# Performance work log

Measured on AMD Instinct MI355X. Metric: run time of the kernel, lower is better.

Reference implementation:

```python
import jax, jax.numpy as jnp
import numpy as np

TOP_K = 2  # num_active_experts


def setup_inputs() -> dict:
    key = jax.random.key(0)
    k1, k2, k3 = jax.random.split(key, 3)
    N, D, E = 16384, 1024, 8
    x = jax.random.normal(k1, (N, D), dtype=jnp.float32)
    router_w = jax.random.normal(k2, (E, D), dtype=jnp.float32) * (1.0 / np.sqrt(D))
    router_b = jnp.zeros((E,), dtype=jnp.float32)
    expert_w = jax.random.normal(k3, (E, D, D), dtype=jnp.float32) * (1.0 / np.sqrt(D))
    expert_b = jnp.zeros((E, D), dtype=jnp.float32)
    return {"x": x, "router_w": router_w, "router_b": router_b,
            "expert_w": expert_w, "expert_b": expert_b}


def reference(x, router_w, router_b, expert_w, expert_b):
    E = router_w.shape[0]
    # Router: softmax over experts, pick top-k, renormalize
    logits = x @ router_w.T + router_b                      # [N, E]
    probs = jax.nn.softmax(logits, axis=-1)                 # [N, E]
    top_p, top_i = jax.lax.top_k(probs, TOP_K)              # [N, K]
    top_p = top_p / jnp.sum(top_p, axis=-1, keepdims=True)  # renormalized gates
    # Dense combine weights: [N, E], zero for non-selected experts
    combine = jnp.sum(jax.nn.one_hot(top_i, E, dtype=x.dtype) * top_p[..., None], axis=1)
    # All-expert outputs, then weighted combine (vectorized dispatch/combine)
    y = jnp.einsum('nd,eod->neo', x, expert_w) + expert_b   # [N, E, O]
    out = jnp.einsum('neo,ne->no', y, combine)              # [N, O]
    return out
```

## Files before the change

kernel.cpp:

```cpp
#include <hip/hip_runtime.h>
#include <hip/hip_bf16.h>


constexpr int DIMS = 1024;
constexpr int NE   = 8;
constexpr int ROUTER_BLOCKS = 1024;
constexpr int WCONV_BLOCKS  = NE * DIMS * DIMS / (8 * 256);

typedef __attribute__((ext_vector_type(8))) short short8;
typedef __attribute__((ext_vector_type(4))) float f32x4;

typedef const __attribute__((address_space(1))) void* gp_t;
typedef __attribute__((address_space(3))) void* sp_t;

__device__ __forceinline__ float b2f(unsigned short u) {
  union { unsigned int i; float f; } x; x.i = ((unsigned)u) << 16; return x.f;
}

__global__ __launch_bounds__(256) void prep_kernel(
    const float* __restrict__ x, const float* __restrict__ rw,
    const float* __restrict__ rb, const float* __restrict__ ew,
    __hip_bfloat16* __restrict__ xb, __hip_bfloat16* __restrict__ wb,
    int* __restrict__ counts, int* __restrict__ entries,
    float* __restrict__ gates, int n_tok) {
  const int tid = threadIdx.x;

  if ((int)blockIdx.x >= ROUTER_BLOCKS) {
    size_t i = (size_t)(blockIdx.x - ROUTER_BLOCKS) * 256 + tid;
    const float4* w4 = (const float4*)ew;
    float4 a = w4[i * 2], b = w4[i * 2 + 1];
    union { __hip_bfloat16 h[8]; float4 f; } u;
    u.h[0] = __float2bfloat16(a.x); u.h[1] = __float2bfloat16(a.y);
    u.h[2] = __float2bfloat16(a.z); u.h[3] = __float2bfloat16(a.w);
    u.h[4] = __float2bfloat16(b.x); u.h[5] = __float2bfloat16(b.y);
    u.h[6] = __float2bfloat16(b.z); u.h[7] = __float2bfloat16(b.w);
    ((float4*)wb)[i] = u.f;
    return;
  }

  __shared__ float s_rw[NE * DIMS];
  __shared__ int s_cnt[NE], s_base[NE];
  __shared__ int s_e[32];
  __shared__ float s_g[32];
  __shared__ int s_pos[32];

  const float4* rw4 = (const float4*)rw;
  float4* s4 = (float4*)s_rw;
  for (int i = tid; i < NE * DIMS / 4; i += 256) s4[i] = rw4[i];
  if (tid < NE) s_cnt[tid] = 0;
  __syncthreads();

  const int wave = tid >> 6, lane = tid & 63;
  for (int i = 0; i < 4; ++i) {
    int t = blockIdx.x * 16 + wave * 4 + i;
    float a[NE];
#pragma unroll
    for (int e = 0; e < NE; ++e) a[e] = 0.f;
#pragma unroll
    for (int j = 0; j < DIMS / 64; ++j) {
      int d = lane + j * 64;
      float v = x[(size_t)t * DIMS + d];
      xb[(size_t)t * DIMS + d] = __float2bfloat16(v);
#pragma unroll
      for (int e = 0; e < NE; ++e) a[e] = fmaf(v, s_rw[e * DIMS + d], a[e]);
    }
    double da[NE];
#pragma unroll
    for (int e = 0; e < NE; ++e) da[e] = (double)a[e];
#pragma unroll
    for (int off = 32; off > 0; off >>= 1) {
#pragma unroll
      for (int e = 0; e < NE; ++e) da[e] += __shfl_xor(da[e], off, 64);
    }
    if (lane == 0) {
      float l[NE];
#pragma unroll
      for (int e = 0; e < NE; ++e) l[e] = (float)da[e] + rb[e];
      int e0 = 0;
#pragma unroll
      for (int e = 1; e < NE; ++e) if (l[e] > l[e0]) e0 = e;
      int e1 = (e0 == 0) ? 1 : 0;
#pragma unroll
      for (int e = 0; e < NE; ++e) if (e != e0 && l[e] > l[e1]) e1 = e;
      float r = expf(l[e1] - l[e0]);
      float g0 = 1.f / (1.f + r);
      float g1 = 1.f - g0;
      int ai = (wave * 4 + i) * 2;
      int p0 = atomicAdd(&s_cnt[e0], 1);
      int p1 = atomicAdd(&s_cnt[e1], 1);
      s_e[ai] = e0; s_g[ai] = g0; s_pos[ai] = p0;
      s_e[ai + 1] = e1; s_g[ai + 1] = g1; s_pos[ai + 1] = p1;
    }
  }
  __syncthreads();
  if (tid < NE) s_base[tid] = atomicAdd(&counts[tid], s_cnt[tid]);
  __syncthreads();
  if (tid < 32) {
    int e = s_e[tid];
    int p = s_base[e] + s_pos[tid];
    int tok = blockIdx.x * 16 + (tid >> 1);
    entries[e * n_tok + p] = (tok << 1) | (tid & 1);
    gates[e * n_tok + p] = s_g[tid];
  }
}

__global__ __launch_bounds__(256) void moe_gemm(
    const __hip_bfloat16* __restrict__ xb, const __hip_bfloat16* __restrict__ wb,
    const float* __restrict__ eb, const int* __restrict__ counts,
    const int* __restrict__ entries, const float* __restrict__ gates,
    __hip_bfloat16* __restrict__ y, int n_tok) {
  int e = -1, rt = 0, cnt = 0, acc_t = 0;
#pragma unroll
  for (int i = 0; i < NE; ++i) {
    int c = counts[i];
    int t = (c + 127) >> 7;
    if (e < 0 && (int)blockIdx.y < acc_t + t) { e = i; rt = (int)blockIdx.y - acc_t; cnt = c; }
    acc_t += t;
  }
  if (e < 0) return;

  __shared__ __hip_bfloat16 As[2][128 * 32];
  __shared__ __hip_bfloat16 Bs[2][128 * 32];

  const int tid = threadIdx.x;
  const int lane = tid & 63, wave = tid >> 6;
  const int row0 = rt * 128;
  const int n0 = blockIdx.x * 128;

  const int rA0 = tid >> 2, rA1 = rA0 + 64;
  const int kcol = (tid & 3) * 8;
  int gr0 = row0 + rA0, gr1 = row0 + rA1;
  int ent0 = (gr0 < cnt) ? entries[e * n_tok + gr0] : 0;
  int ent1 = (gr1 < cnt) ? entries[e * n_tok + gr1] : 0;
  const __hip_bfloat16* ap0 = xb + (size_t)(ent0 >> 1) * DIMS + kcol;
  const __hip_bfloat16* ap1 = xb + (size_t)(ent1 >> 1) * DIMS + kcol;
  const __hip_bfloat16* wbase = wb + (size_t)e * DIMS * DIMS;
  const __hip_bfloat16* bp0 = wbase + (size_t)(n0 + rA0) * DIMS + kcol;
  const __hip_bfloat16* bp1 = wbase + (size_t)(n0 + rA1) * DIMS + kcol;

  f32x4 acc[4][4] = {};

  const int wm = (wave & 1) * 64, wn = (wave >> 1) * 64;
  const int fr = lane & 15, fko = (lane >> 4) * 8;

  for (int k0 = 0; k0 < DIMS; k0 += 64) {
#pragma unroll
    for (int s = 0; s < 2; ++s) {
      __builtin_amdgcn_global_load_lds((gp_t)(ap0 + k0 + s * 32), (sp_t)(As[s] + tid * 8), 16, 0, 0);
      __builtin_amdgcn_global_load_lds((gp_t)(ap1 + k0 + s * 32), (sp_t)(As[s] + (tid + 256) * 8), 16, 0, 0);
      __builtin_amdgcn_global_load_lds((gp_t)(bp0 + k0 + s * 32), (sp_t)(Bs[s] + tid * 8), 16, 0, 0);
      __builtin_amdgcn_global_load_lds((gp_t)(bp1 + k0 + s * 32), (sp_t)(Bs[s] + (tid + 256) * 8), 16, 0, 0);
    }
    __syncthreads();
#pragma unroll
    for (int s = 0; s < 2; ++s) {
      short8 af[4], bf[4];
#pragma unroll
      for (int mt = 0; mt < 4; ++mt)
        af[mt] = *(const short8*)&As[s][(wm + mt * 16 + fr) * 32 + fko];
#pragma unroll
      for (int nt = 0; nt < 4; ++nt)
        bf[nt] = *(const short8*)&Bs[s][(wn + nt * 16 + fr) * 32 + fko];
#pragma unroll
      for (int mt = 0; mt < 4; ++mt)
#pragma unroll
        for (int nt = 0; nt < 4; ++nt)
          acc[mt][nt] = __builtin_amdgcn_mfma_f32_16x16x32_bf16(af[mt], bf[nt], acc[mt][nt], 0, 0, 0);
    }
    __syncthreads();
  }

  const int quad = lane >> 4;
  float bias[4];
#pragma unroll
  for (int nt = 0; nt < 4; ++nt) bias[nt] = eb[e * DIMS + n0 + wn + nt * 16 + fr];
#pragma unroll
  for (int mt = 0; mt < 4; ++mt) {
#pragma unroll
    for (int r = 0; r < 4; ++r) {
      int m = wm + mt * 16 + quad * 4 + r;
      int gr = row0 + m;
      if (gr < cnt) {
        int ent = entries[e * n_tok + gr];
        float g = gates[e * n_tok + gr];
        __hip_bfloat16* yp = y + (size_t)ent * DIMS + n0 + wn + fr;
#pragma unroll
        for (int nt = 0; nt < 4; ++nt)
          yp[nt * 16] = __float2bfloat16(g * (acc[mt][nt][r] + bias[nt]));
      }
    }
  }
}

__global__ __launch_bounds__(256) void combine_kernel(const __hip_bfloat16* __restrict__ y,
                                                      float* __restrict__ out) {
  size_t idx = (size_t)blockIdx.x * 256 + threadIdx.x;
  size_t n = idx >> 7;
  int c = (int)(idx & 127) << 3;
  short8 v0 = *(const short8*)(y + (n * 2) * DIMS + c);
  short8 v1 = *(const short8*)(y + (n * 2 + 1) * DIMS + c);
  float4 o0, o1;
  o0.x = b2f((unsigned short)v0[0]) + b2f((unsigned short)v1[0]);
  o0.y = b2f((unsigned short)v0[1]) + b2f((unsigned short)v1[1]);
  o0.z = b2f((unsigned short)v0[2]) + b2f((unsigned short)v1[2]);
  o0.w = b2f((unsigned short)v0[3]) + b2f((unsigned short)v1[3]);
  o1.x = b2f((unsigned short)v0[4]) + b2f((unsigned short)v1[4]);
  o1.y = b2f((unsigned short)v0[5]) + b2f((unsigned short)v1[5]);
  o1.z = b2f((unsigned short)v0[6]) + b2f((unsigned short)v1[6]);
  o1.w = b2f((unsigned short)v0[7]) + b2f((unsigned short)v1[7]);
  float* op = out + n * DIMS + c;
  ((float4*)op)[0] = o0;
  ((float4*)op)[1] = o1;
}

extern "C" void kernel_launch(void* const* d_in, const int* in_sizes, int n_in,
                              void* d_out, int out_size, void* d_ws, size_t ws_size,
                              hipStream_t stream) {
  const float* x  = (const float*)d_in[0];
  const float* rw = (const float*)d_in[1];
  const float* rb = (const float*)d_in[2];
  const float* ew = (const float*)d_in[3];
  const float* eb = (const float*)d_in[4];
  float* out = (float*)d_out;
  const int n_tok = in_sizes[0] / DIMS;

  char* ws = (char*)d_ws;
  size_t off = 0;
  int* counts = (int*)ws;                      off += 256;
  __hip_bfloat16* xb = (__hip_bfloat16*)(ws + off); off += (size_t)n_tok * DIMS * 2;
  __hip_bfloat16* wb = (__hip_bfloat16*)(ws + off); off += (size_t)NE * DIMS * DIMS * 2;
  int*   entries = (int*)(ws + off);           off += (size_t)NE * n_tok * 4;
  float* gates   = (float*)(ws + off);         off += (size_t)NE * n_tok * 4;
  __hip_bfloat16* y = (__hip_bfloat16*)(ws + off); off += (size_t)n_tok * 2 * DIMS * 2;
  if (ws_size < off) return;

  hipMemsetAsync(counts, 0, 256, stream);
  prep_kernel<<<ROUTER_BLOCKS + WCONV_BLOCKS, 256, 0, stream>>>(
      x, rw, rb, ew, xb, wb, counts, entries, gates, n_tok);
  dim3 g(DIMS / 128, 2 * n_tok / 128 + NE);
  moe_gemm<<<g, 256, 0, stream>>>(xb, wb, eb, counts, entries, gates, y, n_tok);
  combine_kernel<<<(unsigned)((size_t)n_tok * DIMS / 8 / 256), 256, 0, stream>>>(y, out);
}
```

Baseline: 301.0 us.

## Enlarge MoE GEMM M-tile to 256 with swizzled LDS and vectorize router

The grouped expert GEMM moves from 128x128 tiles with a 64-wide K step to 256x128 tiles with a 32-wide K step. Each wave now owns 128x64 of output (8x4 MFMA tiles), and LDS reads use an XOR swizzle on the K column to avoid bank conflicts. The larger M tile is meant to cut weight reloads and raise MFMA work per byte loaded, at the cost of more accumulator registers and fewer blocks per expert, with launch_bounds set to 2 blocks per CU. The router pass now loads x as float4, writes packed bf16x4, and reduces the logits in float instead of double.

```diff
diff --git a/kernel.cpp b/kernel.cpp
--- a/kernel.cpp
+++ b/kernel.cpp
@@ -8,6 +8,7 @@
 constexpr int WCONV_BLOCKS  = NE * DIMS * DIMS / (8 * 256);
 
 typedef __attribute__((ext_vector_type(8))) short short8;
+typedef __attribute__((ext_vector_type(4))) short short4_t;
 typedef __attribute__((ext_vector_type(4))) float f32x4;
 
 typedef const __attribute__((address_space(1))) void* gp_t;
@@ -15,6 +16,10 @@
 
 __device__ __forceinline__ float b2f(unsigned short u) {
   union { unsigned int i; float f; } x; x.i = ((unsigned)u) << 16; return x.f;
+}
+__device__ __forceinline__ short f2bs(float f) {
+  __hip_bfloat16 h = __float2bfloat16(f);
+  return *(short*)&h;
 }
 
 __global__ __launch_bounds__(256) void prep_kernel(
@@ -44,38 +49,42 @@
   __shared__ float s_g[32];
   __shared__ int s_pos[32];
 
-  const float4* rw4 = (const float4*)rw;
+  const float4* rw4g = (const float4*)rw;
   float4* s4 = (float4*)s_rw;
-  for (int i = tid; i < NE * DIMS / 4; i += 256) s4[i] = rw4[i];
+  for (int i = tid; i < NE * DIMS / 4; i += 256) s4[i] = rw4g[i];
   if (tid < NE) s_cnt[tid] = 0;
   __syncthreads();
 
+  const float4* s_rw4 = (const float4*)s_rw;
   const int wave = tid >> 6, lane = tid & 63;
   for (int i = 0; i < 4; ++i) {
     int t = blockIdx.x * 16 + wave * 4 + i;
+    const float4* xr = (const float4*)(x + (size_t)t * DIMS);
+    short4_t* xw = (short4_t*)(xb + (size_t)t * DIMS);
     float a[NE];
 #pragma unroll
     for (int e = 0; e < NE; ++e) a[e] = 0.f;
 #pragma unroll
-    for (int j = 0; j < DIMS / 64; ++j) {
-      int d = lane + j * 64;
-      float v = x[(size_t)t * DIMS + d];
-      xb[(size_t)t * DIMS + d] = __float2bfloat16(v);
-#pragma unroll
-      for (int e = 0; e < NE; ++e) a[e] = fmaf(v, s_rw[e * DIMS + d], a[e]);
-    }
-    double da[NE];
-#pragma unroll
-    for (int e = 0; e < NE; ++e) da[e] = (double)a[e];
+    for (int j = 0; j < 4; ++j) {
+      float4 v = xr[lane + j * 64];
+      short4_t p;
+      p[0] = f2bs(v.x); p[1] = f2bs(v.y); p[2] = f2bs(v.z); p[3] = f2bs(v.w);
+      xw[lane + j * 64] = p;
+#pragma unroll
+      for (int e = 0; e < NE; ++e) {
+        float4 w = s_rw4[e * 256 + lane + j * 64];
+        a[e] = fmaf(v.x, w.x, fmaf(v.y, w.y, fmaf(v.z, w.z, fmaf(v.w, w.w, a[e]))));
+      }
+    }
 #pragma unroll
     for (int off = 32; off > 0; off >>= 1) {
 #pragma unroll
-      for (int e = 0; e < NE; ++e) da[e] += __shfl_xor(da[e], off, 64);
+      for (int e = 0; e < NE; ++e) a[e] += __shfl_xor(a[e], off, 64);
     }
     if (lane == 0) {
       float l[NE];
 #pragma unroll
-      for (int e = 0; e < NE; ++e) l[e] = (float)da[e] + rb[e];
+      for (int e = 0; e < NE; ++e) l[e] = a[e] + rb[e];
       int e0 = 0;
 #pragma unroll
       for (int e = 1; e < NE; ++e) if (l[e] > l[e0]) e0 = e;
@@ -104,7 +113,7 @@
   }
 }
 
-__global__ __launch_bounds__(256) void moe_gemm(
+__global__ __launch_bounds__(256, 2) void moe_gemm(
     const __hip_bfloat16* __restrict__ xb, const __hip_bfloat16* __restrict__ wb,
     const float* __restrict__ eb, const int* __restrict__ counts,
     const int* __restrict__ entries, const float* __restrict__ gates,
@@ -113,69 +122,69 @@
 #pragma unroll
   for (int i = 0; i < NE; ++i) {
     int c = counts[i];
-    int t = (c + 127) >> 7;
+    int t = (c + 255) >> 8;
     if (e < 0 && (int)blockIdx.y < acc_t + t) { e = i; rt = (int)blockIdx.y - acc_t; cnt = c; }
     acc_t += t;
   }
   if (e < 0) return;
 
-  __shared__ __hip_bfloat16 As[2][128 * 32];
-  __shared__ __hip_bfloat16 Bs[2][128 * 32];
+  __shared__ __hip_bfloat16 As[256 * 32];
+  __shared__ __hip_bfloat16 Bs[128 * 32];
 
   const int tid = threadIdx.x;
   const int lane = tid & 63, wave = tid >> 6;
-  const int row0 = rt * 128;
+  const int row0 = rt * 256;
   const int n0 = blockIdx.x * 128;
 
-  const int rA0 = tid >> 2, rA1 = rA0 + 64;
-  const int kcol = (tid & 3) * 8;
-  int gr0 = row0 + rA0, gr1 = row0 + rA1;
-  int ent0 = (gr0 < cnt) ? entries[e * n_tok + gr0] : 0;
-  int ent1 = (gr1 < cnt) ? entries[e * n_tok + gr1] : 0;
-  const __hip_bfloat16* ap0 = xb + (size_t)(ent0 >> 1) * DIMS + kcol;
-  const __hip_bfloat16* ap1 = xb + (size_t)(ent1 >> 1) * DIMS + kcol;
+  const int srow = tid >> 2;
+  const int kc = (tid & 3) ^ (srow & 3);
+  const int kcol = kc * 8;
+
+  const __hip_bfloat16* ap[4];
+#pragma unroll
+  for (int i = 0; i < 4; ++i) {
+    int gr = row0 + srow + 64 * i;
+    int ent = (gr < cnt) ? entries[e * n_tok + gr] : 0;
+    ap[i] = xb + (size_t)(ent >> 1) * DIMS + kcol;
+  }
   const __hip_bfloat16* wbase = wb + (size_t)e * DIMS * DIMS;
-  const __hip_bfloat16* bp0 = wbase + (size_t)(n0 + rA0) * DIMS + kcol;
-  const __hip_bfloat16* bp1 = wbase + (size_t)(n0 + rA1) * DIMS + kcol;
-
-  f32x4 acc[4][4] = {};
-
-  const int wm = (wave & 1) * 64, wn = (wave >> 1) * 64;
-  const int fr = lane & 15, fko = (lane >> 4) * 8;
-
-  for (int k0 = 0; k0 < DIMS; k0 += 64) {
-#pragma unroll
-    for (int s = 0; s < 2; ++s) {
-      __builtin_amdgcn_global_load_lds((gp_t)(ap0 + k0 + s * 32), (sp_t)(As[s] + tid * 8), 16, 0, 0);
-      __builtin_amdgcn_global_load_lds((gp_t)(ap1 + k0 + s * 32), (sp_t)(As[s] + (tid + 256) * 8), 16, 0, 0);
-      __builtin_amdgcn_global_load_lds((gp_t)(bp0 + k0 + s * 32), (sp_t)(Bs[s] + tid * 8), 16, 0, 0);
-      __builtin_amdgcn_global_load_lds((gp_t)(bp1 + k0 + s * 32), (sp_t)(Bs[s] + (tid + 256) * 8), 16, 0, 0);
-    }
+  const __hip_bfloat16* bp0 = wbase + (size_t)(n0 + srow) * DIMS + kcol;
+  const __hip_bfloat16* bp1 = wbase + (size_t)(n0 + srow + 64) * DIMS + kcol;
+
+  f32x4 acc[8][4] = {};
+
+  const int wm = (wave & 1) * 128, wn = (wave >> 1) * 64;
+  const int fr = lane & 15, quad = lane >> 4;
+  const int swo = (quad ^ (fr & 3)) * 8;
+
+  for (int k0 = 0; k0 < DIMS; k0 += 32) {
+    __builtin_amdgcn_global_load_lds((gp_t)(ap[0] + k0), (sp_t)(As + tid * 8), 16, 0, 0);
+    __builtin_amdgcn_global_load_lds((gp_t)(ap[1] + k0), (sp_t)(As + (tid + 256) * 8), 16, 0, 0);
+    __builtin_amdgcn_global_load_lds((gp_t)(ap[2] + k0), (sp_t)(As + (tid + 512) * 8), 16, 0, 0);
+    __builtin_amdgcn_global_load_lds((gp_t)(ap[3] + k0), (sp_t)(As + (tid + 768) * 8), 16, 0, 0);
+    __builtin_amdgcn_global_load_lds((gp_t)(bp0 + k0), (sp_t)(Bs + tid * 8), 16, 0, 0);
+    __builtin_amdgcn_global_load_lds((gp_t)(bp1 + k0), (sp_t)(Bs + (tid + 256) * 8), 16, 0, 0);
     __syncthreads();
-#pragma unroll
-    for (int s = 0; s < 2; ++s) {
-      short8 af[4], bf[4];
-#pragma unroll
-      for (int mt = 0; mt < 4; ++mt)
-        af[mt] = *(const short8*)&As[s][(wm + mt * 16 + fr) * 32 + fko];
+    short8 af[8], bf[4];
+#pragma unroll
+    for (int mt = 0; mt < 8; ++mt)
+      af[mt] = *(const short8*)&As[(wm + mt * 16 + fr) * 32 + swo];
+#pragma unroll
+    for (int nt = 0; nt < 4; ++nt)
+      bf[nt] = *(const short8*)&Bs[(wn + nt * 16 + fr) * 32 + swo];
+#pragma unroll
+    for (int mt = 0; mt < 8; ++mt)
 #pragma unroll
       for (int nt = 0; nt < 4; ++nt)
-        bf[nt] = *(const short8*)&Bs[s][(wn + nt * 16 + fr) * 32 + fko];
-#pragma unroll
-      for (int mt = 0; mt < 4; ++mt)
-#pragma unroll
-        for (int nt = 0; nt < 4; ++nt)
-          acc[mt][nt] = __builtin_amdgcn_mfma_f32_16x16x32_bf16(af[mt], bf[nt], acc[mt][nt], 0, 0, 0);
-    }
+        acc[mt][nt] = __builtin_amdgcn_mfma_f32_16x16x32_bf16(af[mt], bf[nt], acc[mt][nt], 0, 0, 0);
     __syncthreads();
   }
 
-  const int quad = lane >> 4;
   float bias[4];
 #pragma unroll
   for (int nt = 0; nt < 4; ++nt) bias[nt] = eb[e * DIMS + n0 + wn + nt * 16 + fr];
 #pragma unroll
-  for (int mt = 0; mt < 4; ++mt) {
+  for (int mt = 0; mt < 8; ++mt) {
 #pragma unroll
     for (int r = 0; r < 4; ++r) {
       int m = wm + mt * 16 + quad * 4 + r;
@@ -237,7 +246,7 @@
   hipMemsetAsync(counts, 0, 256, stream);
   prep_kernel<<<ROUTER_BLOCKS + WCONV_BLOCKS, 256, 0, stream>>>(
       x, rw, rb, ew, xb, wb, counts, entries, gates, n_tok);
-  dim3 g(DIMS / 128, 2 * n_tok / 128 + NE);
+  dim3 g(DIMS / 128, 2 * n_tok / 256 + NE);
   moe_gemm<<<g, 256, 0, stream>>>(xb, wb, eb, counts, entries, gates, y, n_tok);
   combine_kernel<<<(unsigned)((size_t)n_tok * DIMS / 8 / 256), 256, 0, stream>>>(y, out);
 }
```

Result: no change. 301.8 us (+0.3%).
